# Performance work log

Hardware: AMD Instinct MI355X
Metric: run time of the kernel (lower is better)

Reference implementation:

```python
import jax, jax.numpy as jnp
import numpy as np

ROWS, COLS, N_CHARS = 384, 768, 69  # CHARSET length = 69
CH, CW = 28, 14  # char tile height, width


def setup_inputs() -> dict:
    key = jax.random.key(0)
    k1, k2 = jax.random.split(key)
    grid_logits = jax.random.normal(k1, (ROWS, COLS, N_CHARS), dtype=jnp.float32)
    # font rasterizations are in [0, 1] (pixel intensity / 255)
    font = jax.random.uniform(k2, (N_CHARS, CH, CW), dtype=jnp.float32)
    return {"grid_logits": grid_logits, "font": font}


def reference(grid_logits, font):
    rows, cols, n_chars = grid_logits.shape
    ch, cw = font.shape[1], font.shape[2]
    # softmax over characters per grid cell
    probs = jax.nn.softmax(grid_logits, axis=-1)  # (R, C, N)
    # soft blend of font tiles: (R, C, ch, cw)
    soft_tiles = jnp.einsum('rcn,nhw->rchw', probs, font)
    # assemble full image: equivalent to nested torch.cat over rows/cols
    soft_image = soft_tiles.transpose(0, 2, 1, 3).reshape(rows * ch, cols * cw)
    return soft_image[None, None]  # (1, 1, H, W)
```

## Files before the change

kernel.cpp:

```cpp
#include <hip/hip_runtime.h>
#include <hip/hip_bf16.h>

#define ROWS 384
#define COLS 768
#define NCH  69
#define CH   28
#define CW   14
#define KP   96
#define IMG_W 10752
#define ROW_U 104

typedef __attribute__((ext_vector_type(8))) short bfrag;
typedef __attribute__((ext_vector_type(4))) float f32x4;

__device__ __forceinline__ unsigned bf16bits(float x) {
    unsigned b = __float_as_uint(x);
    b += 0x7FFFu + ((b >> 16) & 1u);
    return b >> 16;
}

__device__ __forceinline__ void lds_fence() {
    asm volatile("s_waitcnt lgkmcnt(0)" ::: "memory");
}

__global__ __launch_bounds__(256)
void font_prep(const float* __restrict__ font, unsigned short* __restrict__ Fh) {
    int idx = blockIdx.x * 256 + threadIdx.x;
    if (idx >= CH * 16 * KP) return;
    int k  = idx % KP;
    int hw = idx / KP;
    int w  = hw % 16, h = hw / 16;
    float v = (w < CW && k < NCH) ? font[k * (CH * CW) + h * CW + w] : 0.f;
    Fh[idx] = (unsigned short)bf16bits(v);
}

__global__ __launch_bounds__(128)
void diffrender_v5(const float* __restrict__ logits,
                   const unsigned short* __restrict__ Fh,
                   float* __restrict__ out)
{
    __shared__ __align__(16) unsigned short smem[2][64 * ROW_U];

    const int tid  = threadIdx.x;
    const int lane = tid & 63;
    const int wv   = tid >> 6;
    const int cell = blockIdx.x * 128 + tid;
    const int r    = blockIdx.x / 6;
    const int cb   = (blockIdx.x % 6) * 128;

    const float* lp = logits + (size_t)cell * NCH;
    float e[NCH];
    float m = -INFINITY;
#pragma unroll
    for (int n = 0; n < NCH; ++n) { e[n] = lp[n]; m = fmaxf(m, e[n]); }
    float s = 0.f;
#pragma unroll
    for (int n = 0; n < NCH; ++n) { e[n] = __expf(e[n] - m); s += e[n]; }
    const float inv = 1.f / s;

    unsigned* prow = (unsigned*)&smem[wv][(size_t)lane * ROW_U];
#pragma unroll
    for (int i = 0; i < 34; ++i)
        prow[i] = bf16bits(e[2 * i] * inv) | (bf16bits(e[2 * i + 1] * inv) << 16);
    prow[34] = bf16bits(e[68] * inv);
#pragma unroll
    for (int i = 35; i < 48; ++i) prow[i] = 0;
    lds_fence();

    const int w15   = lane & 15;
    const int kgrp  = (lane >> 4) * 8;
    const int crow4 = (lane >> 4) * 4;
    bfrag a[4][3];
#pragma unroll
    for (int mt = 0; mt < 4; ++mt)
#pragma unroll
        for (int ks = 0; ks < 3; ++ks)
            a[mt][ks] = *(const bfrag*)&smem[wv][(size_t)(mt * 16 + w15) * ROW_U + ks * 32 + kgrp];
    lds_fence();

    float* stage = (float*)&smem[wv][0];

    const unsigned short* fb = Fh + (size_t)w15 * KP + kgrp;
    bfrag bcur[3], bnxt[3];
#pragma unroll
    for (int ks = 0; ks < 3; ++ks)
        bcur[ks] = *(const bfrag*)(fb + ks * 32);

    for (int h = 0; h < CH; ++h) {
        if (h + 1 < CH) {
            const unsigned short* fn = fb + (size_t)(h + 1) * 16 * KP;
#pragma unroll
            for (int ks = 0; ks < 3; ++ks)
                bnxt[ks] = *(const bfrag*)(fn + ks * 32);
        }

        f32x4 acc[4] = {f32x4{0,0,0,0}, f32x4{0,0,0,0}, f32x4{0,0,0,0}, f32x4{0,0,0,0}};
#pragma unroll
        for (int mt = 0; mt < 4; ++mt)
#pragma unroll
            for (int ks = 0; ks < 3; ++ks)
                acc[mt] = __builtin_amdgcn_mfma_f32_16x16x32_bf16(a[mt][ks], bcur[ks], acc[mt], 0, 0, 0);

        if (w15 < CW) {
#pragma unroll
            for (int mt = 0; mt < 4; ++mt)
#pragma unroll
                for (int j = 0; j < 4; ++j)
                    stage[(mt * 16 + crow4 + j) * CW + w15] = acc[mt][j];
        }
        lds_fence();

        float2* o2 = (float2*)(out + (size_t)(r * CH + h) * IMG_W + (size_t)(cb + wv * 64) * CW);
        const float2* s2 = (const float2*)stage;
#pragma unroll
        for (int i = 0; i < 7; ++i)
            o2[i * 64 + lane] = s2[i * 64 + lane];
        lds_fence();

#pragma unroll
        for (int ks = 0; ks < 3; ++ks) bcur[ks] = bnxt[ks];
    }
}

extern "C" void kernel_launch(void* const* d_in, const int* in_sizes, int n_in,
                              void* d_out, int out_size, void* d_ws, size_t ws_size,
                              hipStream_t stream) {
    const float* logits = (const float*)d_in[0];
    const float* font   = (const float*)d_in[1];
    float* out          = (float*)d_out;
    unsigned short* Fh  = (unsigned short*)d_ws;

    font_prep<<<(CH * 16 * KP + 255) / 256, 256, 0, stream>>>(font, Fh);

    const int blocks = (ROWS * COLS) / 128;
    diffrender_v5<<<blocks, 128, 0, stream>>>(logits, Fh, out);
}
```

Before: 124.0 us.

## Process two font rows per iteration, drop LDS fences, widen stores to float4

The main loop now computes two output image rows per iteration, with eight accumulators and doubled B-fragment prefetch. Results are staged for both rows and written with float4 instead of float2 stores. The explicit s_waitcnt LDS fences are removed, leaving intra-wave LDS ordering to hardware and compiler, and the launch bounds now ask for 3 blocks per CU. The aim is fewer loop iterations and sync stalls plus wider stores for this store-bound kernel, at the cost of more registers and reliance on implicit intra-wave LDS ordering.

```diff
diff --git a/kernel.cpp b/kernel.cpp
--- a/kernel.cpp
+++ b/kernel.cpp
@@ -19,10 +19,6 @@
     return b >> 16;
 }
 
-__device__ __forceinline__ void lds_fence() {
-    asm volatile("s_waitcnt lgkmcnt(0)" ::: "memory");
-}
-
 __global__ __launch_bounds__(256)
 void font_prep(const float* __restrict__ font, unsigned short* __restrict__ Fh) {
     int idx = blockIdx.x * 256 + threadIdx.x;
@@ -34,8 +30,8 @@
     Fh[idx] = (unsigned short)bf16bits(v);
 }
 
-__global__ __launch_bounds__(128)
-void diffrender_v5(const float* __restrict__ logits,
+__global__ __launch_bounds__(128, 3)
+void diffrender_v6(const float* __restrict__ logits,
                    const unsigned short* __restrict__ Fh,
                    float* __restrict__ out)
 {
@@ -65,7 +61,6 @@
     prow[34] = bf16bits(e[68] * inv);
 #pragma unroll
     for (int i = 35; i < 48; ++i) prow[i] = 0;
-    lds_fence();
 
     const int w15   = lane & 15;
     const int kgrp  = (lane >> 4) * 8;
@@ -76,49 +71,71 @@
 #pragma unroll
         for (int ks = 0; ks < 3; ++ks)
             a[mt][ks] = *(const bfrag*)&smem[wv][(size_t)(mt * 16 + w15) * ROW_U + ks * 32 + kgrp];
-    lds_fence();
 
     float* stage = (float*)&smem[wv][0];
 
     const unsigned short* fb = Fh + (size_t)w15 * KP + kgrp;
-    bfrag bcur[3], bnxt[3];
+    bfrag bcur[2][3], bnxt[2][3];
 #pragma unroll
-    for (int ks = 0; ks < 3; ++ks)
-        bcur[ks] = *(const bfrag*)(fb + ks * 32);
+    for (int hh = 0; hh < 2; ++hh)
+#pragma unroll
+        for (int ks = 0; ks < 3; ++ks)
+            bcur[hh][ks] = *(const bfrag*)(fb + (size_t)(hh * 16) * KP + ks * 32);
 
-    for (int h = 0; h < CH; ++h) {
-        if (h + 1 < CH) {
-            const unsigned short* fn = fb + (size_t)(h + 1) * 16 * KP;
+#pragma unroll 1
+    for (int h2 = 0; h2 < CH / 2; ++h2) {
+        const int h = 2 * h2;
+        if (h2 + 1 < CH / 2) {
+            const unsigned short* fn = fb + (size_t)((h + 2) * 16) * KP;
 #pragma unroll
-            for (int ks = 0; ks < 3; ++ks)
-                bnxt[ks] = *(const bfrag*)(fn + ks * 32);
+            for (int hh = 0; hh < 2; ++hh)
+#pragma unroll
+                for (int ks = 0; ks < 3; ++ks)
+                    bnxt[hh][ks] = *(const bfrag*)(fn + (size_t)(hh * 16) * KP + ks * 32);
         }
 
-        f32x4 acc[4] = {f32x4{0,0,0,0}, f32x4{0,0,0,0}, f32x4{0,0,0,0}, f32x4{0,0,0,0}};
+        f32x4 acc[2][4];
 #pragma unroll
-        for (int mt = 0; mt < 4; ++mt)
+        for (int hh = 0; hh < 2; ++hh)
 #pragma unroll
-            for (int ks = 0; ks < 3; ++ks)
-                acc[mt] = __builtin_amdgcn_mfma_f32_16x16x32_bf16(a[mt][ks], bcur[ks], acc[mt], 0, 0, 0);
+            for (int mt = 0; mt < 4; ++mt)
+                acc[hh][mt] = f32x4{0, 0, 0, 0};
+#pragma unroll
+        for (int hh = 0; hh < 2; ++hh)
+#pragma unroll
+            for (int mt = 0; mt < 4; ++mt)
+#pragma unroll
+                for (int ks = 0; ks < 3; ++ks)
+                    acc[hh][mt] = __builtin_amdgcn_mfma_f32_16x16x32_bf16(
+                        a[mt][ks], bcur[hh][ks], acc[hh][mt], 0, 0, 0);
 
         if (w15 < CW) {
 #pragma unroll
-            for (int mt = 0; mt < 4; ++mt)
+            for (int hh = 0; hh < 2; ++hh)
 #pragma unroll
-                for (int j = 0; j < 4; ++j)
-                    stage[(mt * 16 + crow4 + j) * CW + w15] = acc[mt][j];
+                for (int mt = 0; mt < 4; ++mt)
+#pragma unroll
+                    for (int j = 0; j < 4; ++j)
+                        stage[hh * 896 + (mt * 16 + crow4 + j) * CW + w15] = acc[hh][mt][j];
         }
-        lds_fence();
-
-        float2* o2 = (float2*)(out + (size_t)(r * CH + h) * IMG_W + (size_t)(cb + wv * 64) * CW);
-        const float2* s2 = (const float2*)stage;
-#pragma unroll
-        for (int i = 0; i < 7; ++i)
-            o2[i * 64 + lane] = s2[i * 64 + lane];
-        lds_fence();
 
 #pragma unroll
-        for (int ks = 0; ks < 3; ++ks) bcur[ks] = bnxt[ks];
+        for (int hh = 0; hh < 2; ++hh) {
+            float4* o4 = (float4*)(out + (size_t)(r * CH + h + hh) * IMG_W
+                                       + (size_t)(cb + wv * 64) * CW);
+            const float4* s4 = (const float4*)(stage + hh * 896);
+#pragma unroll
+            for (int i = 0; i < 4; ++i) {
+                const int idx = i * 64 + lane;
+                if (idx < 224) o4[idx] = s4[idx];
+            }
+        }
+
+#pragma unroll
+        for (int hh = 0; hh < 2; ++hh)
+#pragma unroll
+            for (int ks = 0; ks < 3; ++ks)
+                bcur[hh][ks] = bnxt[hh][ks];
     }
 }
 
@@ -133,5 +150,5 @@
     font_prep<<<(CH * 16 * KP + 255) / 256, 256, 0, stream>>>(font, Fh);
 
     const int blocks = (ROWS * COLS) / 128;
-    diffrender_v5<<<blocks, 128, 0, stream>>>(logits, Fh, out);
+    diffrender_v6<<<blocks, 128, 0, stream>>>(logits, Fh, out);
 }
```

Result: no change. 122.0 us (-1.6%).

## Swap MFMA operand roles to write output directly, drop LDS staging

Applied to the files above, without the earlier changes.

Swaps the A/B operands of the MFMA so the accumulator layout puts four consecutive output-width pixels in each lane. Results can then be stored straight to global memory as float2 pairs, with no LDS staging transpose and no waitcnt fences. Blocks shrink to a single 64-lane wave, and the h loop is unrolled by two. In exchange the global stores are narrower and less coalesced (8-byte pieces spread across cells), and one-wave blocks raise the block count and scheduling overhead.

```diff
diff --git a/kernel.cpp b/kernel.cpp
--- a/kernel.cpp
+++ b/kernel.cpp
@@ -19,10 +19,6 @@
     return b >> 16;
 }
 
-__device__ __forceinline__ void lds_fence() {
-    asm volatile("s_waitcnt lgkmcnt(0)" ::: "memory");
-}
-
 __global__ __launch_bounds__(256)
 void font_prep(const float* __restrict__ font, unsigned short* __restrict__ Fh) {
     int idx = blockIdx.x * 256 + threadIdx.x;
@@ -34,19 +30,18 @@
     Fh[idx] = (unsigned short)bf16bits(v);
 }
 
-__global__ __launch_bounds__(128)
-void diffrender_v5(const float* __restrict__ logits,
+__global__ __launch_bounds__(64)
+void diffrender_v8(const float* __restrict__ logits,
                    const unsigned short* __restrict__ Fh,
                    float* __restrict__ out)
 {
-    __shared__ __align__(16) unsigned short smem[2][64 * ROW_U];
+    __shared__ __align__(16) unsigned short Pa[64 * ROW_U];
 
-    const int tid  = threadIdx.x;
-    const int lane = tid & 63;
-    const int wv   = tid >> 6;
-    const int cell = blockIdx.x * 128 + tid;
-    const int r    = blockIdx.x / 6;
-    const int cb   = (blockIdx.x % 6) * 128;
+    const int lane = threadIdx.x;
+    const int bid  = blockIdx.x;
+    const int r    = bid / 12;
+    const int cb   = (bid % 12) * 64;
+    const int cell = bid * 64 + lane;
 
     const float* lp = logits + (size_t)cell * NCH;
     float e[NCH];
@@ -58,40 +53,37 @@
     for (int n = 0; n < NCH; ++n) { e[n] = __expf(e[n] - m); s += e[n]; }
     const float inv = 1.f / s;
 
-    unsigned* prow = (unsigned*)&smem[wv][(size_t)lane * ROW_U];
+    unsigned* prow = (unsigned*)&Pa[(size_t)lane * ROW_U];
 #pragma unroll
     for (int i = 0; i < 34; ++i)
         prow[i] = bf16bits(e[2 * i] * inv) | (bf16bits(e[2 * i + 1] * inv) << 16);
     prow[34] = bf16bits(e[68] * inv);
 #pragma unroll
     for (int i = 35; i < 48; ++i) prow[i] = 0;
-    lds_fence();
 
-    const int w15   = lane & 15;
+    const int c15   = lane & 15;
     const int kgrp  = (lane >> 4) * 8;
     const int crow4 = (lane >> 4) * 4;
-    bfrag a[4][3];
+    bfrag b[4][3];
 #pragma unroll
     for (int mt = 0; mt < 4; ++mt)
 #pragma unroll
         for (int ks = 0; ks < 3; ++ks)
-            a[mt][ks] = *(const bfrag*)&smem[wv][(size_t)(mt * 16 + w15) * ROW_U + ks * 32 + kgrp];
-    lds_fence();
+            b[mt][ks] = *(const bfrag*)&Pa[(size_t)(mt * 16 + c15) * ROW_U + ks * 32 + kgrp];
 
-    float* stage = (float*)&smem[wv][0];
-
-    const unsigned short* fb = Fh + (size_t)w15 * KP + kgrp;
-    bfrag bcur[3], bnxt[3];
+    const unsigned short* fb = Fh + (size_t)c15 * KP + kgrp;
+    bfrag acur[3], anxt[3];
 #pragma unroll
     for (int ks = 0; ks < 3; ++ks)
-        bcur[ks] = *(const bfrag*)(fb + ks * 32);
+        acur[ks] = *(const bfrag*)(fb + ks * 32);
 
+#pragma unroll 2
     for (int h = 0; h < CH; ++h) {
         if (h + 1 < CH) {
             const unsigned short* fn = fb + (size_t)(h + 1) * 16 * KP;
 #pragma unroll
             for (int ks = 0; ks < 3; ++ks)
-                bnxt[ks] = *(const bfrag*)(fn + ks * 32);
+                anxt[ks] = *(const bfrag*)(fn + ks * 32);
         }
 
         f32x4 acc[4] = {f32x4{0,0,0,0}, f32x4{0,0,0,0}, f32x4{0,0,0,0}, f32x4{0,0,0,0}};
@@ -99,26 +91,19 @@
         for (int mt = 0; mt < 4; ++mt)
 #pragma unroll
             for (int ks = 0; ks < 3; ++ks)
-                acc[mt] = __builtin_amdgcn_mfma_f32_16x16x32_bf16(a[mt][ks], bcur[ks], acc[mt], 0, 0, 0);
+                acc[mt] = __builtin_amdgcn_mfma_f32_16x16x32_bf16(acur[ks], b[mt][ks], acc[mt], 0, 0, 0);
 
-        if (w15 < CW) {
+        float* orow = out + (size_t)(r * CH + h) * IMG_W;
 #pragma unroll
-            for (int mt = 0; mt < 4; ++mt)
-#pragma unroll
-                for (int j = 0; j < 4; ++j)
-                    stage[(mt * 16 + crow4 + j) * CW + w15] = acc[mt][j];
+        for (int mt = 0; mt < 4; ++mt) {
+            float* p = orow + (size_t)(cb + mt * 16 + c15) * CW + crow4;
+            *(float2*)p = make_float2(acc[mt][0], acc[mt][1]);
+            if (crow4 < 12)
+                *(float2*)(p + 2) = make_float2(acc[mt][2], acc[mt][3]);
         }
-        lds_fence();
-
-        float2* o2 = (float2*)(out + (size_t)(r * CH + h) * IMG_W + (size_t)(cb + wv * 64) * CW);
-        const float2* s2 = (const float2*)stage;
-#pragma unroll
-        for (int i = 0; i < 7; ++i)
-            o2[i * 64 + lane] = s2[i * 64 + lane];
-        lds_fence();
 
 #pragma unroll
-        for (int ks = 0; ks < 3; ++ks) bcur[ks] = bnxt[ks];
+        for (int ks = 0; ks < 3; ++ks) acur[ks] = anxt[ks];
     }
 }
 
@@ -132,6 +117,6 @@
 
     font_prep<<<(CH * 16 * KP + 255) / 256, 256, 0, stream>>>(font, Fh);
 
-    const int blocks = (ROWS * COLS) / 128;
-    diffrender_v5<<<blocks, 128, 0, stream>>>(logits, Fh, out);
+    const int blocks = (ROWS * COLS) / 64;
+    diffrender_v8<<<blocks, 64, 0, stream>>>(logits, Fh, out);
 }
```

Result: slower. 137.1 us (+10.6%).
